# Kernel optimization log

Hardware: AMD Instinct MI355X
Metric: run time of the kernel (lower is better)

## Reference

```python
import jax, jax.numpy as jnp
import numpy as np

DIM = 2048
N_HEADS = 32
N_KV_HEADS = 8
HEAD_DIM = DIM // N_HEADS  # 64
N_REP = N_HEADS // N_KV_HEADS  # 4
B, S = 2, 2048
MASK_VAL = -32768.0


def setup_inputs() -> dict:
    key = jax.random.key(0)
    ks = jax.random.split(key, 7)
    x = jax.random.normal(ks[0], (B, S, DIM), dtype=jnp.float32)
    freqs_cos = jax.random.uniform(ks[1], (S, HEAD_DIM // 2), dtype=jnp.float32)
    freqs_sin = jax.random.uniform(ks[2], (S, HEAD_DIM // 2), dtype=jnp.float32)
    sc = 1.0 / np.sqrt(DIM)
    wq = jax.random.normal(ks[3], (N_HEADS * HEAD_DIM, DIM), dtype=jnp.float32) * sc
    wk = jax.random.normal(ks[4], (N_KV_HEADS * HEAD_DIM, DIM), dtype=jnp.float32) * sc
    wv = jax.random.normal(ks[5], (N_KV_HEADS * HEAD_DIM, DIM), dtype=jnp.float32) * sc
    wo = jax.random.normal(ks[6], (DIM, N_HEADS * HEAD_DIM), dtype=jnp.float32) * sc
    return {"x": x, "freqs_cos": freqs_cos, "freqs_sin": freqs_sin,
            "wq": wq, "wk": wk, "wv": wv, "wo": wo}


def _apply_rope(q, k, cos, sin):
    # q: [B,S,H,D], k: [B,S,Hkv,D]; interleaved real/imag pairs in last dim
    def rot(t):
        tr = t.reshape(t.shape[:-1] + (-1, 2))  # [..., D/2, 2]
        t_r, t_i = tr[..., 0], tr[..., 1]
        c = cos[None, :, None, :]  # broadcast over batch and heads
        s = sin[None, :, None, :]
        o_r = t_r * c - t_i * s
        o_i = t_r * s + t_i * c
        return jnp.stack([o_r, o_i], axis=-1).reshape(t.shape)
    return rot(q), rot(k)


def reference(x, freqs_cos, freqs_sin, wq, wk, wv, wo):
    bsz, seqlen, _ = x.shape
    xq = (x @ wq.T).reshape(bsz, seqlen, N_HEADS, HEAD_DIM)
    xk = (x @ wk.T).reshape(bsz, seqlen, N_KV_HEADS, HEAD_DIM)
    xv = (x @ wv.T).reshape(bsz, seqlen, N_KV_HEADS, HEAD_DIM)
    xq, xk = _apply_rope(xq, xk, freqs_cos, freqs_sin)
    # GQA: repeat each kv head n_rep times contiguously (matches per-head cat loop)
    xk = jnp.repeat(xk, N_REP, axis=2)  # [B,S,H,D]
    xv = jnp.repeat(xv, N_REP, axis=2)
    # [B,H,S,D]
    q = xq.transpose(0, 2, 1, 3)
    k = xk.transpose(0, 2, 1, 3)
    v = xv.transpose(0, 2, 1, 3)
    scores = jnp.einsum('bhqd,bhkd->bhqk', q, k) / jnp.sqrt(jnp.float32(HEAD_DIM))
    causal = jnp.triu(jnp.full((seqlen, seqlen), MASK_VAL, dtype=scores.dtype), k=1)
    scores = scores + causal[None, None, :, :]
    probs = jax.nn.softmax(scores.astype(jnp.float32), axis=-1).astype(q.dtype)
    out = jnp.einsum('bhqk,bhkd->bhqd', probs, v)
    out = out.transpose(0, 2, 1, 3).reshape(bsz, seqlen, -1)
    return out @ wo.T
```

## Files before the change

### kernel.cpp

```cpp
#include <hip/hip_runtime.h>
#include <hip/hip_bf16.h>
#include <type_traits>

typedef __bf16 bf16;
typedef __bf16 bf16x2 __attribute__((ext_vector_type(2)));
typedef __bf16 bf16x4 __attribute__((ext_vector_type(4)));
typedef __bf16 bf16x8 __attribute__((ext_vector_type(8)));
typedef float f32x4 __attribute__((ext_vector_type(4)));

#define AS1 __attribute__((address_space(1)))
#define AS3 __attribute__((address_space(3)))

#define KAPPA 0.180336880111f

__device__ __forceinline__ void load_lds16(const void* g, void* l) {
  __builtin_amdgcn_global_load_lds((AS1 void*)g, (AS3 void*)l, 16, 0, 0);
}
__device__ __forceinline__ float exp2_fast(float x) {
  return __builtin_amdgcn_exp2f(x);
}

__global__ void f2b_all(const float* __restrict__ x, const float* __restrict__ wq,
                        const float* __restrict__ wk, const float* __restrict__ wv,
                        const float* __restrict__ wo, bf16* __restrict__ xb,
                        bf16* __restrict__ wqkv, bf16* __restrict__ wob) {
  int bid = blockIdx.x;
  const float* src;
  bf16* dst;
  int nblk, kblk, nb;
  if (bid < 4096) {
    nblk = bid >> 6;
    kblk = bid & 63;
    src = x;
    nb = nblk * 64;
    dst = xb;
  } else if (bid < 7168) {
    int b2 = bid - 4096;
    nblk = b2 >> 6;
    kblk = b2 & 63;
    int n0 = nblk * 64;
    if (n0 < 2048) { src = wq; nb = n0; }
    else if (n0 < 2560) { src = wk; nb = n0 - 2048; }
    else { src = wv; nb = n0 - 2560; }
    dst = wqkv;
  } else {
    int b3 = bid - 7168;
    nblk = b3 >> 6;
    kblk = b3 & 63;
    src = wo;
    nb = nblk * 64;
    dst = wob;
  }
  const int t = threadIdx.x, j = t >> 6, l = t & 63;
  const int n = nb + j * 16 + (l & 15);
  const int k = kblk * 32 + (l >> 4) * 8;
  float4 v0 = *(const float4*)(src + (size_t)n * 2048 + k);
  float4 v1 = *(const float4*)(src + (size_t)n * 2048 + k + 4);
  bf16x8 o = {(bf16)v0.x, (bf16)v0.y, (bf16)v0.z, (bf16)v0.w,
              (bf16)v1.x, (bf16)v1.y, (bf16)v1.z, (bf16)v1.w};
  *(bf16x8*)((char*)dst + ((size_t)(nblk * 64 + kblk)) * 4096 + j * 1024 +
             l * 16) = o;
}

__global__ __launch_bounds__(256, 3) void gemm_qkv(const bf16* __restrict__ A,
                                                   const bf16* __restrict__ Bw,
                                                   const float* __restrict__ fc,
                                                   const float* __restrict__ fs,
                                                   bf16* __restrict__ Qro,
                                                   bf16* __restrict__ Kro,
                                                   bf16* __restrict__ Vt) {
  const int t = threadIdx.x;
  const int wave = t >> 6, lane = t & 63, qd = lane >> 4, ln = lane & 15;
  const int wm = (wave >> 1) * 64;
  const int wn = (wave & 1) * 64;
  const int bn = blockIdx.x;
  const size_t bm = (size_t)blockIdx.y * 128;

  const int mblk0 = (int)(blockIdx.y * 2) + (wm >> 6);
  const char* Aw = (const char*)A + (size_t)mblk0 * 262144 + (size_t)lane * 16;
  const int n0 = bn * 2 + (wn >> 6);
  const char* Bb = (const char*)Bw + (size_t)n0 * 262144 + (size_t)lane * 16;

  f32x4 acc[4][4] = {};
  bf16x8 a0[4], b0[4], a1[4], b1[4];

  auto loadT = [&](int tk, bf16x8 (&a)[4], bf16x8 (&b)[4]) {
#pragma unroll
    for (int i = 0; i < 4; i++)
      a[i] = *(const bf16x8*)(Aw + (size_t)tk * 4096 + i * 1024);
#pragma unroll
    for (int j = 0; j < 4; j++)
      b[j] = *(const bf16x8*)(Bb + (size_t)tk * 4096 + j * 1024);
  };

  loadT(0, a0, b0);
  loadT(1, a1, b1);

  auto step = [&](int tk, bf16x8 (&ca)[4], bf16x8 (&cb)[4]) {
    __builtin_amdgcn_s_setprio(1);
#pragma unroll
    for (int i = 0; i < 4; i++)
#pragma unroll
      for (int j = 0; j < 4; j++)
        acc[i][j] = __builtin_amdgcn_mfma_f32_16x16x32_bf16(ca[i], cb[j],
                                                            acc[i][j], 0, 0, 0);
    __builtin_amdgcn_s_setprio(0);
    if (tk + 2 < 64) loadT(tk + 2, ca, cb);
  };

#pragma unroll 1
  for (int tk = 0; tk < 64; tk += 2) {
    step(tk, a0, b0);
    step(tk + 1, a1, b1);
  }

  const int b = (int)(bm >> 11);
  const int sb = (int)(bm & 2047) + wm;
  const bool odd = ln & 1;

  if (bn < 20) {
    const bool isQ = bn < 16;
    const float kap = isQ ? KAPPA : 1.0f;
    const int hh = isQ ? (bn * 2 + (wn >> 6)) : ((bn - 16) * 2 + (wn >> 6));
    bf16* dst = isQ ? (Qro + ((size_t)(b * 32 + hh) * 2048) * 64)
                    : (Kro + ((size_t)(b * 8 + hh) * 2048) * 64);
#pragma unroll
    for (int i = 0; i < 4; i++) {
#pragma unroll
      for (int j = 0; j < 4; j++) {
        const int d = j * 16 + ln;
        const int i_f = d >> 1;
#pragma unroll
        for (int r = 0; r < 4; r++) {
          int s = sb + i * 16 + qd * 4 + r;
          float v = acc[i][j][r];
          float p = __shfl_xor(v, 1);
          float cv = fc[s * 32 + i_f] * kap;
          float sv = fs[s * 32 + i_f] * kap;
          float o = odd ? (p * sv + v * cv) : (v * cv - p * sv);
          dst[(size_t)s * 64 + d] = (bf16)o;
        }
      }
    }
  } else {
    const int kh = (bn - 20) * 2 + (wn >> 6);
#pragma unroll
    for (int i = 0; i < 4; i++)
#pragma unroll
      for (int j = 0; j < 4; j++) {
        const int d = j * 16 + ln;
        int s = sb + i * 16 + qd * 4;
        bf16x4 ov = {(bf16)acc[i][j][0], (bf16)acc[i][j][1],
                     (bf16)acc[i][j][2], (bf16)acc[i][j][3]};
        *(bf16x4*)&Vt[((size_t)(b * 8 + kh) * 64 + d) * 2048 + s] = ov;
      }
  }
}

__global__ __launch_bounds__(256, 4) void gemm_bt(const bf16* __restrict__ A,
                                                  const bf16* __restrict__ Bw,
                                                  float* __restrict__ C) {
  const int K = 2048, N = 2048;
  __shared__ bf16 As[3][64][32];
  const int t = threadIdx.x;
  const int wave = t >> 6, lane = t & 63, qd = lane >> 4, ln = lane & 15;
  const int wm = (wave >> 1) * 32;
  const int wn = (wave & 1) * 64;
  const size_t bm = (size_t)blockIdx.y * 64;
  const size_t bn = (size_t)blockIdx.x * 128;

  const bf16* Ab = A + bm * (size_t)K;
  const int n0 = (int)(bn >> 6) + (wn >> 6);
  const char* Bb = (const char*)Bw + (size_t)n0 * 262144 + (size_t)lane * 16;

  auto stage = [&](int tk, int slot) {
    int ro = t >> 2, gs = (t & 3) ^ ((ro >> 1) & 3);
    load_lds16(Ab + (size_t)ro * K + tk * 32 + gs * 8,
               (char*)As + slot * 4096 + wave * 1024);
  };

  f32x4 acc[2][4] = {};
  const int segoff = (qd ^ ((ln >> 1) & 3)) << 4;
  bf16x8 b0[4], b1[4];

#pragma unroll
  for (int j = 0; j < 4; j++)
    b0[j] = *(const bf16x8*)(Bb + (size_t)j * 1024);
  stage(0, 0);
  stage(1, 1);
  asm volatile("s_waitcnt vmcnt(1)" ::: "memory");
  __builtin_amdgcn_s_barrier();

  auto step = [&](int tk, bf16x8 (&cb)[4], bf16x8 (&nb)[4]) {
    if (tk < 62) stage(tk + 2, (tk + 2) % 3);
    if (tk < 63) {
#pragma unroll
      for (int j = 0; j < 4; j++)
        nb[j] = *(const bf16x8*)(Bb + (size_t)(tk + 1) * 4096 + j * 1024);
    }
    const char* Asl = (const char*)As + (tk % 3) * 4096;
    bf16x8 af[2];
#pragma unroll
    for (int i = 0; i < 2; i++)
      af[i] = *(const bf16x8*)(Asl + (wm + i * 16 + ln) * 64 + segoff);
    if (tk <= 61) asm volatile("s_waitcnt lgkmcnt(0) vmcnt(5)" ::: "memory");
    else if (tk == 62) asm volatile("s_waitcnt lgkmcnt(0) vmcnt(4)" ::: "memory");
    else asm volatile("s_waitcnt lgkmcnt(0) vmcnt(0)" ::: "memory");
    __builtin_amdgcn_sched_barrier(0);
    __builtin_amdgcn_s_setprio(1);
#pragma unroll
    for (int i = 0; i < 2; i++)
#pragma unroll
      for (int j = 0; j < 4; j++)
        acc[i][j] = __builtin_amdgcn_mfma_f32_16x16x32_bf16(af[i], cb[j],
                                                            acc[i][j], 0, 0, 0);
    __builtin_amdgcn_s_setprio(0);
    if (tk < 63) __builtin_amdgcn_s_barrier();
  };

  for (int tk = 0; tk < 64; tk += 2) {
    step(tk, b0, b1);
    step(tk + 1, b1, b0);
  }

#pragma unroll
  for (int i = 0; i < 2; i++)
#pragma unroll
    for (int j = 0; j < 4; j++)
#pragma unroll
      for (int r = 0; r < 4; r++) {
        size_t row = bm + wm + i * 16 + qd * 4 + r;
        size_t col = bn + wn + j * 16 + ln;
        C[row * N + col] = acc[i][j][r];
      }
}

__global__ __launch_bounds__(256, 3) void attn_fwd(const bf16* __restrict__ Q,
                                                   const bf16* __restrict__ Kg,
                                                   const bf16* __restrict__ Vg,
                                                   bf16* __restrict__ O) {
  __shared__ bf16 Ks[2][64][64];
  __shared__ bf16 Vs[2][64][64];
  __shared__ bf16 Ps[128][64];
  const int t = threadIdx.x;
  const int wave = t >> 6, lane = t & 63, qd = lane >> 4, ln = lane & 15;
  const int bid = blockIdx.x;
  const int qt = 15 - (bid >> 6);
  const int bh = bid & 63;
  const int b = bh >> 5, h = bh & 31, kh = h >> 2;
  const bf16* Qb = Q + ((size_t)(b * 32 + h) * 2048 + qt * 128) * 64;
  const bf16* Kb = Kg + (size_t)(b * 8 + kh) * 2048 * 64;
  const bf16* Vb = Vg + (size_t)(b * 8 + kh) * 64 * 2048;
  char* PsB = (char*)Ps;

  bf16x8 qf[2][2];
#pragma unroll
  for (int kk = 0; kk < 2; kk++)
#pragma unroll
    for (int mi = 0; mi < 2; mi++)
      qf[kk][mi] = *(const bf16x8*)(Qb + (wave * 32 + mi * 16 + ln) * 64 +
                                    (kk * 4 + qd) * 8);

  auto stageKV = [&](int kb, int buf) {
#pragma unroll
    for (int i = 0; i < 2; i++) {
      int e = i * 256 + t;
      int row = e >> 3, sg = (e & 7) ^ (row & 7);
      load_lds16(Kb + (size_t)(kb * 64 + row) * 64 + sg * 8,
                 (char*)Ks + buf * 8192 + i * 4096 + wave * 1024);
      load_lds16(Vb + (size_t)row * 2048 + kb * 64 + sg * 8,
                 (char*)Vs + buf * 8192 + i * 4096 + wave * 1024);
    }
  };

  f32x4 o_acc[4][2] = {};
  float l_st[2] = {0.f, 0.f};
  const int q0 = qt * 128 + wave * 32;
  const int nkb = 2 * qt + 2;

  stageKV(0, 0);
  __syncthreads();

  for (int kb = 0; kb < nkb; kb++) {
    const int cur = kb & 1;
    if (kb + 1 < nkb) stageKV(kb + 1, cur ^ 1);
    const char* Ksl = (const char*)Ks + cur * 8192;
    const char* Vsl = (const char*)Vs + cur * 8192;

    f32x4 s_acc[4][2] = {};
#pragma unroll
    for (int kk = 0; kk < 2; kk++) {
      bf16x8 ak[4];
#pragma unroll
      for (int j = 0; j < 4; j++) {
        int row = j * 16 + ln;
        int ph = (kk * 4 + qd) ^ (ln & 7);
        ak[j] = *(const bf16x8*)(Ksl + row * 128 + ph * 16);
      }
#pragma unroll
      for (int j = 0; j < 4; j++)
#pragma unroll
        for (int mi = 0; mi < 2; mi++)
          s_acc[j][mi] = __builtin_amdgcn_mfma_f32_16x16x32_bf16(
              ak[j], qf[kk][mi], s_acc[j][mi], 0, 0, 0);
    }

    auto smax = [&](auto maskc) {
      constexpr bool MASK = decltype(maskc)::value;
#pragma unroll
      for (int mi = 0; mi < 2; mi++) {
        const int qv = q0 + mi * 16 + ln;
        const int prow = wave * 32 + mi * 16 + ln;
        float rs = 0.f;
#pragma unroll
        for (int j = 0; j < 4; j++) {
          bf16x4 pk;
#pragma unroll
          for (int r = 0; r < 4; r++) {
            float s = s_acc[j][mi][r];
            if (MASK) {
              int k_glob = kb * 64 + j * 16 + qd * 4 + r;
              if (k_glob > qv) s = -1e5f;
            }
            float pv = exp2_fast(s - 16.f);
            rs += pv;
            pk[r] = (bf16)pv;
          }
          int ps = (j * 2 + (qd >> 1)) ^ (ln & 7);
          *(bf16x4*)(PsB + prow * 128 + ps * 16 + (qd & 1) * 8) = pk;
        }
        l_st[mi] += rs;
      }
    };
    if (kb * 64 + 63 > q0) smax(std::true_type{});
    else smax(std::false_type{});

#pragma unroll
    for (int kk = 0; kk < 2; kk++) {
      bf16x8 av[4], bp[2];
#pragma unroll
      for (int dj = 0; dj < 4; dj++) {
        int row = dj * 16 + ln;
        int ph = (kk * 4 + qd) ^ (ln & 7);
        av[dj] = *(const bf16x8*)(Vsl + row * 128 + ph * 16);
      }
#pragma unroll
      for (int mi = 0; mi < 2; mi++) {
        int prow = wave * 32 + mi * 16 + ln;
        int ph = (kk * 4 + qd) ^ (ln & 7);
        bp[mi] = *(const bf16x8*)(PsB + prow * 128 + ph * 16);
      }
#pragma unroll
      for (int dj = 0; dj < 4; dj++)
#pragma unroll
        for (int mi = 0; mi < 2; mi++)
          o_acc[dj][mi] = __builtin_amdgcn_mfma_f32_16x16x32_bf16(
              av[dj], bp[mi], o_acc[dj][mi], 0, 0, 0);
    }

    __syncthreads();
  }

#pragma unroll
  for (int mi = 0; mi < 2; mi++) {
    float lt = l_st[mi];
    lt += __shfl_xor(lt, 16);
    lt += __shfl_xor(lt, 32);
    float inv = 1.f / lt;
    int q_idx = qt * 128 + wave * 32 + mi * 16 + ln;
#pragma unroll
    for (int dj = 0; dj < 4; dj++) {
      bf16x4 ov;
#pragma unroll
      for (int r = 0; r < 4; r++) ov[r] = (bf16)(o_acc[dj][mi][r] * inv);
      *(bf16x4*)&O[((size_t)(b * 2048 + q_idx) * 32 + h) * 64 + dj * 16 + qd * 4] = ov;
    }
  }
}

extern "C" void kernel_launch(void* const* d_in, const int* in_sizes, int n_in,
                              void* d_out, int out_size, void* d_ws,
                              size_t ws_size, hipStream_t stream) {
  const float* x = (const float*)d_in[0];
  const float* fc = (const float*)d_in[1];
  const float* fs = (const float*)d_in[2];
  const float* wq = (const float*)d_in[3];
  const float* wk = (const float*)d_in[4];
  const float* wv = (const float*)d_in[5];
  const float* wo = (const float*)d_in[6];
  float* out = (float*)d_out;

  char* ws = (char*)d_ws;
  const size_t MB = (size_t)1 << 20;
  bf16* xb   = (bf16*)(ws + 0 * MB);
  bf16* wqkv = (bf16*)(ws + 16 * MB);
  bf16* wob  = (bf16*)(ws + 28 * MB);
  bf16* Qro  = (bf16*)(ws + 36 * MB);
  bf16* Kro  = (bf16*)(ws + 52 * MB);
  bf16* Vt   = (bf16*)(ws + 56 * MB);
  bf16* Oa   = (bf16*)(ws + 60 * MB);

  dim3 blk(256);
  f2b_all<<<9216, blk, 0, stream>>>(x, wq, wk, wv, wo, xb, wqkv, wob);
  gemm_qkv<<<dim3(24, 32), blk, 0, stream>>>(xb, wqkv, fc, fs, Qro, Kro, Vt);
  attn_fwd<<<1024, blk, 0, stream>>>(Qro, Kro, Vt, Oa);
  gemm_bt<<<dim3(16, 64), blk, 0, stream>>>(Oa, wob, out);
}
```

Before: 288.4 us.

## Stage QKV weight tiles through swizzled LDS and store weights row-major

The QKV weight conversion now writes wq/wk/wv as plain row-major bf16 instead of the MFMA-tiled layout, using a simple elementwise cast. The QKV GEMM now loads B tiles into a triple-buffered XOR-swizzled LDS ring with global_load_lds, shared across all four waves. Each wave now covers 32 rows by 128 columns instead of 64 by 64, with A fragments read directly from global memory. The goal is to cut redundant global weight traffic and make the conversion pass cheaper, at the cost of per-step barriers and LDS reads.

```diff
diff --git a/kernel.cpp b/kernel.cpp
--- a/kernel.cpp
+++ b/kernel.cpp
@@ -25,34 +25,37 @@
                         const float* __restrict__ wo, bf16* __restrict__ xb,
                         bf16* __restrict__ wqkv, bf16* __restrict__ wob) {
   int bid = blockIdx.x;
+  if (bid >= 4096 && bid < 10240) {
+    int b2 = bid - 4096;
+    const float* src;
+    bf16* dst = wqkv;
+    int off;
+    if (b2 < 4096) { src = wq; off = b2; }
+    else if (b2 < 5120) { src = wk; dst = wqkv + 4194304; off = b2 - 4096; }
+    else { src = wv; dst = wqkv + 5242880; off = b2 - 5120; }
+    int i = (off * 256 + threadIdx.x) * 4;
+    float4 v = *(const float4*)(src + i);
+    bf16x4 o = {(bf16)v.x, (bf16)v.y, (bf16)v.z, (bf16)v.w};
+    *(bf16x4*)(dst + i) = o;
+    return;
+  }
   const float* src;
   bf16* dst;
-  int nblk, kblk, nb;
+  int nblk, kblk;
   if (bid < 4096) {
     nblk = bid >> 6;
     kblk = bid & 63;
     src = x;
-    nb = nblk * 64;
     dst = xb;
-  } else if (bid < 7168) {
-    int b2 = bid - 4096;
-    nblk = b2 >> 6;
-    kblk = b2 & 63;
-    int n0 = nblk * 64;
-    if (n0 < 2048) { src = wq; nb = n0; }
-    else if (n0 < 2560) { src = wk; nb = n0 - 2048; }
-    else { src = wv; nb = n0 - 2560; }
-    dst = wqkv;
   } else {
-    int b3 = bid - 7168;
+    int b3 = bid - 10240;
     nblk = b3 >> 6;
     kblk = b3 & 63;
     src = wo;
-    nb = nblk * 64;
     dst = wob;
   }
   const int t = threadIdx.x, j = t >> 6, l = t & 63;
-  const int n = nb + j * 16 + (l & 15);
+  const int n = nblk * 64 + j * 16 + (l & 15);
   const int k = kblk * 32 + (l >> 4) * 8;
   float4 v0 = *(const float4*)(src + (size_t)n * 2048 + k);
   float4 v1 = *(const float4*)(src + (size_t)n * 2048 + k + 4);
@@ -69,67 +72,90 @@
                                                    bf16* __restrict__ Qro,
                                                    bf16* __restrict__ Kro,
                                                    bf16* __restrict__ Vt) {
+  const int K = 2048;
+  __shared__ bf16 Bs[3][128][32];
   const int t = threadIdx.x;
   const int wave = t >> 6, lane = t & 63, qd = lane >> 4, ln = lane & 15;
-  const int wm = (wave >> 1) * 64;
-  const int wn = (wave & 1) * 64;
   const int bn = blockIdx.x;
   const size_t bm = (size_t)blockIdx.y * 128;
 
-  const int mblk0 = (int)(blockIdx.y * 2) + (wm >> 6);
-  const char* Aw = (const char*)A + (size_t)mblk0 * 262144 + (size_t)lane * 16;
-  const int n0 = bn * 2 + (wn >> 6);
-  const char* Bb = (const char*)Bw + (size_t)n0 * 262144 + (size_t)lane * 16;
-
-  f32x4 acc[4][4] = {};
-  bf16x8 a0[4], b0[4], a1[4], b1[4];
-
-  auto loadT = [&](int tk, bf16x8 (&a)[4], bf16x8 (&b)[4]) {
-#pragma unroll
-    for (int i = 0; i < 4; i++)
-      a[i] = *(const bf16x8*)(Aw + (size_t)tk * 4096 + i * 1024);
-#pragma unroll
-    for (int j = 0; j < 4; j++)
-      b[j] = *(const bf16x8*)(Bb + (size_t)tk * 4096 + j * 1024);
+  const int mblk = (int)(blockIdx.y * 2) + (wave >> 1);
+  const int j0 = (wave & 1) * 2;
+  const char* Aw = (const char*)A + (size_t)mblk * 262144 +
+                   (size_t)j0 * 1024 + (size_t)lane * 16;
+  const bf16* Bb = Bw + (size_t)bn * 128 * K;
+
+  auto stageB = [&](int tk, int slot) {
+#pragma unroll
+    for (int sub = 0; sub < 2; sub++) {
+      int e = sub * 256 + t;
+      int ro = e >> 2, gs = (e & 3) ^ ((ro >> 1) & 3);
+      load_lds16(Bb + (size_t)ro * K + tk * 32 + gs * 8,
+                 (char*)Bs + slot * 8192 + sub * 4096 + wave * 1024);
+    }
   };
 
-  loadT(0, a0, b0);
-  loadT(1, a1, b1);
-
-  auto step = [&](int tk, bf16x8 (&ca)[4], bf16x8 (&cb)[4]) {
+  f32x4 acc[2][8] = {};
+  const int segoff = (qd ^ ((ln >> 1) & 3)) << 4;
+  bf16x8 a0[2], a1[2];
+
+  stageB(0, 0);
+  stageB(1, 1);
+#pragma unroll
+  for (int i = 0; i < 2; i++)
+    a0[i] = *(const bf16x8*)(Aw + (size_t)i * 1024);
+  asm volatile("s_waitcnt vmcnt(0)" ::: "memory");
+  __builtin_amdgcn_s_barrier();
+
+  auto step = [&](int tk, bf16x8 (&ca)[2], bf16x8 (&na)[2]) {
+    if (tk < 62) stageB(tk + 2, (tk + 2) % 3);
+    if (tk < 63) {
+#pragma unroll
+      for (int i = 0; i < 2; i++)
+        na[i] = *(const bf16x8*)(Aw + (size_t)(tk + 1) * 4096 + i * 1024);
+    }
+    const char* Bsl = (const char*)Bs + (tk % 3) * 8192;
+    bf16x8 bf[8];
+#pragma unroll
+    for (int j = 0; j < 8; j++)
+      bf[j] = *(const bf16x8*)(Bsl + (j * 16 + ln) * 64 + segoff);
+    if (tk <= 61) asm volatile("s_waitcnt lgkmcnt(0) vmcnt(4)" ::: "memory");
+    else if (tk == 62) asm volatile("s_waitcnt lgkmcnt(0) vmcnt(2)" ::: "memory");
+    else asm volatile("s_waitcnt lgkmcnt(0) vmcnt(0)" ::: "memory");
+    __builtin_amdgcn_sched_barrier(0);
     __builtin_amdgcn_s_setprio(1);
 #pragma unroll
-    for (int i = 0; i < 4; i++)
-#pragma unroll
-      for (int j = 0; j < 4; j++)
-        acc[i][j] = __builtin_amdgcn_mfma_f32_16x16x32_bf16(ca[i], cb[j],
+    for (int i = 0; i < 2; i++)
+#pragma unroll
+      for (int j = 0; j < 8; j++)
+        acc[i][j] = __builtin_amdgcn_mfma_f32_16x16x32_bf16(ca[i], bf[j],
                                                             acc[i][j], 0, 0, 0);
     __builtin_amdgcn_s_setprio(0);
-    if (tk + 2 < 64) loadT(tk + 2, ca, cb);
+    if (tk < 63) __builtin_amdgcn_s_barrier();
   };
 
-#pragma unroll 1
   for (int tk = 0; tk < 64; tk += 2) {
-    step(tk, a0, b0);
-    step(tk + 1, a1, b1);
+    step(tk, a0, a1);
+    step(tk + 1, a1, a0);
   }
 
   const int b = (int)(bm >> 11);
-  const int sb = (int)(bm & 2047) + wm;
+  const int sb = (int)(bm & 2047) + wave * 32;
   const bool odd = ln & 1;
 
   if (bn < 20) {
     const bool isQ = bn < 16;
     const float kap = isQ ? KAPPA : 1.0f;
-    const int hh = isQ ? (bn * 2 + (wn >> 6)) : ((bn - 16) * 2 + (wn >> 6));
-    bf16* dst = isQ ? (Qro + ((size_t)(b * 32 + hh) * 2048) * 64)
-                    : (Kro + ((size_t)(b * 8 + hh) * 2048) * 64);
-#pragma unroll
-    for (int i = 0; i < 4; i++) {
-#pragma unroll
-      for (int j = 0; j < 4; j++) {
-        const int d = j * 16 + ln;
-        const int i_f = d >> 1;
+    const int hbase = isQ ? bn * 2 : (bn - 16) * 2;
+#pragma unroll
+    for (int j = 0; j < 8; j++) {
+      const int hh = hbase + (j >> 2);
+      bf16* dst = isQ ? (Qro + ((size_t)(b * 32 + hh) * 2048) * 64)
+                      : (Kro + ((size_t)(b * 8 + hh) * 2048) * 64);
+      const int d = (j & 3) * 16 + ln;
+      const int i_f = d >> 1;
+#pragma unroll
+      for (int i = 0; i < 2; i++) {
 #pragma unroll
         for (int r = 0; r < 4; r++) {
           int s = sb + i * 16 + qd * 4 + r;
@@ -143,17 +169,18 @@
       }
     }
   } else {
-    const int kh = (bn - 20) * 2 + (wn >> 6);
-#pragma unroll
-    for (int i = 0; i < 4; i++)
-#pragma unroll
-      for (int j = 0; j < 4; j++) {
-        const int d = j * 16 + ln;
+#pragma unroll
+    for (int j = 0; j < 8; j++) {
+      const int kh = (bn - 20) * 2 + (j >> 2);
+      const int d = (j & 3) * 16 + ln;
+#pragma unroll
+      for (int i = 0; i < 2; i++) {
         int s = sb + i * 16 + qd * 4;
         bf16x4 ov = {(bf16)acc[i][j][0], (bf16)acc[i][j][1],
                      (bf16)acc[i][j][2], (bf16)acc[i][j][3]};
         *(bf16x4*)&Vt[((size_t)(b * 8 + kh) * 64 + d) * 2048 + s] = ov;
       }
+    }
   }
 }
 
@@ -401,7 +428,7 @@
   bf16* Oa   = (bf16*)(ws + 60 * MB);
 
   dim3 blk(256);
-  f2b_all<<<9216, blk, 0, stream>>>(x, wq, wk, wv, wo, xb, wqkv, wob);
+  f2b_all<<<12288, blk, 0, stream>>>(x, wq, wk, wv, wo, xb, wqkv, wob);
   gemm_qkv<<<dim3(24, 32), blk, 0, stream>>>(xb, wqkv, fc, fs, Qro, Kro, Vt);
   attn_fwd<<<1024, blk, 0, stream>>>(Qro, Kro, Vt, Oa);
   gemm_bt<<<dim3(16, 64), blk, 0, stream>>>(Oa, wob, out);
```

Result: no change. 285.3 us (-1.1%).
